# Kernel optimization log

Measured on AMD Instinct MI355X. Metric: run time of the kernel, lower is better.

The kernel has to match this reference:

```python
import jax, jax.numpy as jnp
import numpy as np

N_NODES = 90  # hard-coded per-graph node count in the original module
HIDDEN = 128


def setup_inputs() -> dict:
    key = jax.random.key(0)
    ks = jax.random.split(key, 12)
    B = 8192
    adj = jax.random.uniform(ks[0], (B, N_NODES, N_NODES), dtype=jnp.float32)
    s_in = 1.0 / np.sqrt(N_NODES)
    s_h = 1.0 / np.sqrt(HIDDEN)
    return {
        "adj": adj,
        "W_mlp0": jax.random.normal(ks[1], (N_NODES, HIDDEN), jnp.float32) * s_in,
        "b_mlp0": jax.random.normal(ks[2], (HIDDEN,), jnp.float32) * s_in,
        "W_mlp1": jax.random.normal(ks[3], (HIDDEN, HIDDEN), jnp.float32) * s_h,
        "b_mlp1": jax.random.normal(ks[4], (HIDDEN,), jnp.float32) * s_h,
        "W_mlp2": jax.random.normal(ks[5], (HIDDEN, HIDDEN), jnp.float32) * s_h,
        "b_mlp2": jax.random.normal(ks[6], (HIDDEN,), jnp.float32) * s_h,
        "W_res1": jax.random.normal(ks[7], (HIDDEN, HIDDEN), jnp.float32) * s_h,
        "b_res1": jax.random.normal(ks[8], (HIDDEN,), jnp.float32) * s_h,
        "W_res2": jax.random.normal(ks[9], (HIDDEN, HIDDEN), jnp.float32) * s_h,
        "b_res2": jax.random.normal(ks[10], (HIDDEN,), jnp.float32) * s_h,
    }


def reference(adj, W_mlp0, b_mlp0, W_mlp1, b_mlp1, W_mlp2, b_mlp2,
              W_res1, b_res1, W_res2, b_res2):
    B = adj.shape[0]
    # raw node features: identity per graph (torch.eye(90) concatenated)
    raw_x = jnp.broadcast_to(jnp.eye(N_NODES, dtype=adj.dtype), (B, N_NODES, N_NODES))

    def gconv(x, W, b):
        # block-diagonal Adj_block @ x == batched per-graph matmul, then linear
        return jnp.einsum('bij,bjk->bik', adj, x) @ W + b

    # encoding == 1 branch, layers = 3
    h0 = gconv(raw_x, W_mlp0, b_mlp0)                    # mlps[0](raw_x, A)
    r1 = h0 @ W_res1 + b_res1                            # res[1](h0)
    x = jax.nn.relu(gconv(h0, W_mlp1, b_mlp1)) + r1      # layer 1
    Y = jax.nn.relu(gconv(x, W_mlp2, b_mlp2) + (r1 @ W_res2 + b_res2))  # final

    # decoder: per-graph inner-product, concatenated along node axis
    Z = jnp.einsum('bik,bjk->bij', Y, Y)                 # [B, 90, 90]
    return Z.reshape(B * N_NODES, N_NODES)
```

## Files before the change

### kernel.cpp

```cpp
#include <hip/hip_runtime.h>
#include <hip/hip_bf16.h>


#define NN 90
#define HH 128
#define NT 256

typedef _Float16 half8 __attribute__((ext_vector_type(8)));
typedef _Float16 half4 __attribute__((ext_vector_type(4)));
typedef float floatx16 __attribute__((ext_vector_type(16)));

#define SR 136
#define SR8 17
#define ST 104
#define ST8 13
#define ST4 26

#define MFMA(a, b, c) __builtin_amdgcn_mfma_f32_32x32x16_f16((a), (b), (c), 0, 0, 0)

__global__ void prep_weights(const float* __restrict__ W0,
                             const float* __restrict__ Wr1,
                             const float* __restrict__ W1,
                             const float* __restrict__ W2,
                             const float* __restrict__ Wr2,
                             _Float16* __restrict__ ws)
{
    const int idx = blockIdx.x * blockDim.x + threadIdx.x;
    if (idx >= 77824) return;
    if (idx < 12288) {
        const int n = idx / 96, k = idx - n * 96;
        ws[idx] = (k < NN) ? (_Float16)W0[k * HH + n] : (_Float16)0.f;
    } else {
        const int j = idx - 12288;
        const int m = j >> 14;
        const int r = j & 16383;
        const int n = r >> 7, k = r & 127;
        const float* src = (m == 0) ? Wr1 : (m == 1) ? W1 : (m == 2) ? W2 : Wr2;
        ws[idx] = (_Float16)src[k * HH + n];
    }
}

__global__ __launch_bounds__(NT) void graphcnn_mfma(
    const float* __restrict__ adj,
    const _Float16* __restrict__ wts,
    const float* __restrict__ b0, const float* __restrict__ b1,
    const float* __restrict__ b2, const float* __restrict__ br1,
    const float* __restrict__ br2,
    float* __restrict__ out)
{
    __shared__ __align__(16) unsigned char smem[98816];
    _Float16* adjH = (_Float16*)smem;
    _Float16* bufA = (_Float16*)(smem + 19968);
    _Float16* bufT = (_Float16*)(smem + 46080);
    _Float16* r1R  = (_Float16*)(smem + 72704);

    const int t    = threadIdx.x;
    const int wv   = t >> 6;
    const int lane = t & 63;
    const int p    = lane & 31;
    const int h    = lane >> 5;
    const int n    = wv * 32 + p;

    const _Float16* W0T  = wts;
    const _Float16* Wr1T = wts + 12288;
    const _Float16* W1T  = Wr1T + 16384;
    const _Float16* W2T  = W1T + 16384;
    const _Float16* Wr2T = W2T + 16384;

    for (int i = t; i < (96 * ST) / 2; i += NT) ((unsigned int*)adjH)[i] = 0u;
    __syncthreads();
    const float* Ag = adj + (size_t)blockIdx.x * (NN * NN);
    for (int i = t; i < NN * NN; i += NT) {
        const int r = i / NN, c = i - r * NN;
        adjH[r * ST + c] = (_Float16)Ag[i];
    }
    __syncthreads();

    auto writeR = [&](_Float16* buf, int mt, int col, const floatx16& A) {
        #pragma unroll
        for (int r = 0; r < 16; r++) {
            const int node = mt * 32 + (r & 3) + 8 * (r >> 2) + 4 * h;
            buf[node * SR + col] = (_Float16)A[r];
        }
    };
    auto writeT = [&](_Float16* buf, int mt, int col, const floatx16& A) {
        #pragma unroll
        for (int rg = 0; rg < 4; rg++) {
            half4 v = { (_Float16)A[4*rg], (_Float16)A[4*rg+1],
                        (_Float16)A[4*rg+2], (_Float16)A[4*rg+3] };
            ((half4*)buf)[col * ST4 + mt * 8 + 2 * rg + h] = v;
        }
    };

    floatx16 acc0, acc1, acc2;

    {
        half8 bf[6];
        #pragma unroll
        for (int kt = 0; kt < 6; kt++) bf[kt] = ((const half8*)W0T)[n * 12 + kt * 2 + h];
        const float bias = b0[n];
        #pragma unroll
        for (int r = 0; r < 16; r++) { acc0[r] = bias; acc1[r] = bias; acc2[r] = bias; }
        #pragma unroll
        for (int kt = 0; kt < 6; kt++) {
            half8 a0 = ((const half8*)adjH)[(0 * 32 + p) * ST8 + kt * 2 + h];
            half8 a1 = ((const half8*)adjH)[(1 * 32 + p) * ST8 + kt * 2 + h];
            half8 a2 = ((const half8*)adjH)[(2 * 32 + p) * ST8 + kt * 2 + h];
            acc0 = MFMA(a0, bf[kt], acc0);
            acc1 = MFMA(a1, bf[kt], acc1);
            acc2 = MFMA(a2, bf[kt], acc2);
        }
        writeR(bufA, 0, n, acc0); writeR(bufA, 1, n, acc1); writeR(bufA, 2, n, acc2);
        writeT(bufT, 0, n, acc0); writeT(bufT, 1, n, acc1); writeT(bufT, 2, n, acc2);
    }
    __syncthreads();

    {
        half8 bf[8];
        #pragma unroll
        for (int kt = 0; kt < 8; kt++) bf[kt] = ((const half8*)Wr1T)[n * 16 + kt * 2 + h];
        const float bias = br1[n];
        #pragma unroll
        for (int r = 0; r < 16; r++) { acc0[r] = bias; acc1[r] = bias; acc2[r] = bias; }
        #pragma unroll
        for (int kt = 0; kt < 8; kt++) {
            half8 a0 = ((const half8*)bufA)[(0 * 32 + p) * SR8 + kt * 2 + h];
            half8 a1 = ((const half8*)bufA)[(1 * 32 + p) * SR8 + kt * 2 + h];
            half8 a2 = ((const half8*)bufA)[(2 * 32 + p) * SR8 + kt * 2 + h];
            acc0 = MFMA(a0, bf[kt], acc0);
            acc1 = MFMA(a1, bf[kt], acc1);
            acc2 = MFMA(a2, bf[kt], acc2);
        }
        writeR(r1R, 0, n, acc0); writeR(r1R, 1, n, acc1); writeR(r1R, 2, n, acc2);
    }
    __syncthreads();

    {
        #pragma unroll
        for (int r = 0; r < 16; r++) { acc0[r] = 0.f; acc1[r] = 0.f; acc2[r] = 0.f; }
        #pragma unroll
        for (int kt = 0; kt < 6; kt++) {
            half8 bfk = ((const half8*)bufT)[n * ST8 + kt * 2 + h];
            half8 a0 = ((const half8*)adjH)[(0 * 32 + p) * ST8 + kt * 2 + h];
            half8 a1 = ((const half8*)adjH)[(1 * 32 + p) * ST8 + kt * 2 + h];
            half8 a2 = ((const half8*)adjH)[(2 * 32 + p) * ST8 + kt * 2 + h];
            acc0 = MFMA(a0, bfk, acc0);
            acc1 = MFMA(a1, bfk, acc1);
            acc2 = MFMA(a2, bfk, acc2);
        }
        writeR(bufA, 0, n, acc0); writeR(bufA, 1, n, acc1); writeR(bufA, 2, n, acc2);
    }
    __syncthreads();

    {
        half8 bf[8];
        #pragma unroll
        for (int kt = 0; kt < 8; kt++) bf[kt] = ((const half8*)W1T)[n * 16 + kt * 2 + h];
        const float bias = b1[n];
        #pragma unroll
        for (int r = 0; r < 16; r++) { acc0[r] = bias; acc1[r] = bias; acc2[r] = bias; }
        #pragma unroll
        for (int kt = 0; kt < 8; kt++) {
            half8 a0 = ((const half8*)bufA)[(0 * 32 + p) * SR8 + kt * 2 + h];
            half8 a1 = ((const half8*)bufA)[(1 * 32 + p) * SR8 + kt * 2 + h];
            half8 a2 = ((const half8*)bufA)[(2 * 32 + p) * SR8 + kt * 2 + h];
            acc0 = MFMA(a0, bf[kt], acc0);
            acc1 = MFMA(a1, bf[kt], acc1);
            acc2 = MFMA(a2, bf[kt], acc2);
        }
        #pragma unroll
        for (int mt = 0; mt < 3; mt++) {
            floatx16& A = (mt == 0) ? acc0 : (mt == 1) ? acc1 : acc2;
            floatx16 xv;
            #pragma unroll
            for (int r = 0; r < 16; r++) {
                const int node = mt * 32 + (r & 3) + 8 * (r >> 2) + 4 * h;
                xv[r] = fmaxf(A[r], 0.f) + (float)r1R[node * SR + n];
            }
            writeT(bufT, mt, n, xv);
        }
    }
    __syncthreads();

    {
        #pragma unroll
        for (int r = 0; r < 16; r++) { acc0[r] = 0.f; acc1[r] = 0.f; acc2[r] = 0.f; }
        #pragma unroll
        for (int kt = 0; kt < 6; kt++) {
            half8 bfk = ((const half8*)bufT)[n * ST8 + kt * 2 + h];
            half8 a0 = ((const half8*)adjH)[(0 * 32 + p) * ST8 + kt * 2 + h];
            half8 a1 = ((const half8*)adjH)[(1 * 32 + p) * ST8 + kt * 2 + h];
            half8 a2 = ((const half8*)adjH)[(2 * 32 + p) * ST8 + kt * 2 + h];
            acc0 = MFMA(a0, bfk, acc0);
            acc1 = MFMA(a1, bfk, acc1);
            acc2 = MFMA(a2, bfk, acc2);
        }
        writeR(bufA, 0, n, acc0); writeR(bufA, 1, n, acc1); writeR(bufA, 2, n, acc2);
    }
    __syncthreads();

    {
        half8 bf[8];
        #pragma unroll
        for (int kt = 0; kt < 8; kt++) bf[kt] = ((const half8*)W2T)[n * 16 + kt * 2 + h];
        const float bias = b2[n] + br2[n];
        #pragma unroll
        for (int r = 0; r < 16; r++) { acc0[r] = bias; acc1[r] = bias; acc2[r] = bias; }
        #pragma unroll
        for (int kt = 0; kt < 8; kt++) {
            half8 a0 = ((const half8*)bufA)[(0 * 32 + p) * SR8 + kt * 2 + h];
            half8 a1 = ((const half8*)bufA)[(1 * 32 + p) * SR8 + kt * 2 + h];
            half8 a2 = ((const half8*)bufA)[(2 * 32 + p) * SR8 + kt * 2 + h];
            acc0 = MFMA(a0, bf[kt], acc0);
            acc1 = MFMA(a1, bf[kt], acc1);
            acc2 = MFMA(a2, bf[kt], acc2);
        }
        half8 bg[8];
        #pragma unroll
        for (int kt = 0; kt < 8; kt++) bg[kt] = ((const half8*)Wr2T)[n * 16 + kt * 2 + h];
        #pragma unroll
        for (int kt = 0; kt < 8; kt++) {
            half8 a0 = ((const half8*)r1R)[(0 * 32 + p) * SR8 + kt * 2 + h];
            half8 a1 = ((const half8*)r1R)[(1 * 32 + p) * SR8 + kt * 2 + h];
            half8 a2 = ((const half8*)r1R)[(2 * 32 + p) * SR8 + kt * 2 + h];
            acc0 = MFMA(a0, bg[kt], acc0);
            acc1 = MFMA(a1, bg[kt], acc1);
            acc2 = MFMA(a2, bg[kt], acc2);
        }
        _Float16* YR = bufT;
        #pragma unroll
        for (int mt = 0; mt < 3; mt++) {
            floatx16& A = (mt == 0) ? acc0 : (mt == 1) ? acc1 : acc2;
            #pragma unroll
            for (int r = 0; r < 16; r++) {
                const int node = mt * 32 + (r & 3) + 8 * (r >> 2) + 4 * h;
                YR[node * SR + n] = (_Float16)fmaxf(A[r], 0.f);
            }
        }
    }
    __syncthreads();

    {
        const _Float16* YR = bufT;
        float* outb = out + (size_t)blockIdx.x * (NN * NN);
        auto ztile = [&](int mt, int nt) {
            floatx16 acc;
            #pragma unroll
            for (int r = 0; r < 16; r++) acc[r] = 0.f;
            #pragma unroll
            for (int kt = 0; kt < 8; kt++) {
                half8 av = ((const half8*)YR)[(mt * 32 + p) * SR8 + kt * 2 + h];
                half8 bv = ((const half8*)YR)[(nt * 32 + p) * SR8 + kt * 2 + h];
                acc = MFMA(av, bv, acc);
            }
            const int col = nt * 32 + p;
            if (col < NN) {
                #pragma unroll
                for (int r = 0; r < 16; r++) {
                    const int row = mt * 32 + (r & 3) + 8 * (r >> 2) + 4 * h;
                    if (row < NN) outb[row * NN + col] = acc[r];
                }
            }
        };
        if      (wv == 0) { ztile(0, 0); ztile(0, 1); ztile(0, 2); }
        else if (wv == 1) { ztile(1, 0); ztile(1, 1); }
        else if (wv == 2) { ztile(1, 2); ztile(2, 0); }
        else              { ztile(2, 1); ztile(2, 2); }
    }
}

extern "C" void kernel_launch(void* const* d_in, const int* in_sizes, int n_in,
                              void* d_out, int out_size, void* d_ws, size_t ws_size,
                              hipStream_t stream) {
    const float* adj = (const float*)d_in[0];
    const float* W0  = (const float*)d_in[1];
    const float* b0  = (const float*)d_in[2];
    const float* W1  = (const float*)d_in[3];
    const float* b1  = (const float*)d_in[4];
    const float* W2  = (const float*)d_in[5];
    const float* b2  = (const float*)d_in[6];
    const float* Wr1 = (const float*)d_in[7];
    const float* br1 = (const float*)d_in[8];
    const float* Wr2 = (const float*)d_in[9];
    const float* br2 = (const float*)d_in[10];
    float* out = (float*)d_out;
    _Float16* wts = (_Float16*)d_ws;

    prep_weights<<<76, 1024, 0, stream>>>(W0, Wr1, W1, W2, Wr2, wts);

    const int B = in_sizes[0] / (NN * NN);
    graphcnn_mfma<<<B, NT, 0, stream>>>(adj, wts, b0, b1, b2, br1, br2, out);
}
```

Baseline: 819.7 us.

## Split per-graph work across 12 waves, one 32-row tile per wave

Raises the block from 4 to 12 waves so each wave owns one 32-row by 32-column output tile instead of three row tiles, and spreads the nine decoder tiles across nine waves. Each matmul now uses two independent accumulator chains to hide MFMA latency. The r1 residual is kept in registers instead of re-read from LDS, and extra barriers are added so in-place buffer overwrites stay safe. The cost is more barriers per stage, launch_bounds(768,3) register pressure, and redundant weight-fragment loads across the three row-tile waves.

```diff
diff --git a/kernel.cpp b/kernel.cpp
--- a/kernel.cpp
+++ b/kernel.cpp
@@ -4,7 +4,7 @@
 
 #define NN 90
 #define HH 128
-#define NT 256
+#define NT 768
 
 typedef _Float16 half8 __attribute__((ext_vector_type(8)));
 typedef _Float16 half4 __attribute__((ext_vector_type(4)));
@@ -40,7 +40,7 @@
     }
 }
 
-__global__ __launch_bounds__(NT) void graphcnn_mfma(
+__global__ __launch_bounds__(NT, 3) void graphcnn_mfma(
     const float* __restrict__ adj,
     const _Float16* __restrict__ wts,
     const float* __restrict__ b0, const float* __restrict__ b1,
@@ -59,7 +59,10 @@
     const int lane = t & 63;
     const int p    = lane & 31;
     const int h    = lane >> 5;
-    const int n    = wv * 32 + p;
+    const int mt   = wv >> 2;
+    const int cg   = wv & 3;
+    const int n    = cg * 32 + p;
+    const int arow = mt * 32 + p;
 
     const _Float16* W0T  = wts;
     const _Float16* Wr1T = wts + 12288;
@@ -76,42 +79,43 @@
     }
     __syncthreads();
 
-    auto writeR = [&](_Float16* buf, int mt, int col, const floatx16& A) {
+    auto ldA = [&](const _Float16* buf, int s8, int kt) {
+        return ((const half8*)buf)[arow * s8 + kt * 2 + h];
+    };
+    auto writeR = [&](_Float16* buf, const floatx16& A) {
         #pragma unroll
         for (int r = 0; r < 16; r++) {
             const int node = mt * 32 + (r & 3) + 8 * (r >> 2) + 4 * h;
-            buf[node * SR + col] = (_Float16)A[r];
+            buf[node * SR + n] = (_Float16)A[r];
         }
     };
-    auto writeT = [&](_Float16* buf, int mt, int col, const floatx16& A) {
+    auto writeT = [&](_Float16* buf, const floatx16& A) {
         #pragma unroll
         for (int rg = 0; rg < 4; rg++) {
             half4 v = { (_Float16)A[4*rg], (_Float16)A[4*rg+1],
                         (_Float16)A[4*rg+2], (_Float16)A[4*rg+3] };
-            ((half4*)buf)[col * ST4 + mt * 8 + 2 * rg + h] = v;
+            ((half4*)buf)[n * ST4 + mt * 8 + 2 * rg + h] = v;
         }
     };
 
-    floatx16 acc0, acc1, acc2;
+    floatx16 r1reg;
 
     {
         half8 bf[6];
         #pragma unroll
         for (int kt = 0; kt < 6; kt++) bf[kt] = ((const half8*)W0T)[n * 12 + kt * 2 + h];
         const float bias = b0[n];
-        #pragma unroll
-        for (int r = 0; r < 16; r++) { acc0[r] = bias; acc1[r] = bias; acc2[r] = bias; }
-        #pragma unroll
-        for (int kt = 0; kt < 6; kt++) {
-            half8 a0 = ((const half8*)adjH)[(0 * 32 + p) * ST8 + kt * 2 + h];
-            half8 a1 = ((const half8*)adjH)[(1 * 32 + p) * ST8 + kt * 2 + h];
-            half8 a2 = ((const half8*)adjH)[(2 * 32 + p) * ST8 + kt * 2 + h];
-            acc0 = MFMA(a0, bf[kt], acc0);
-            acc1 = MFMA(a1, bf[kt], acc1);
-            acc2 = MFMA(a2, bf[kt], acc2);
-        }
-        writeR(bufA, 0, n, acc0); writeR(bufA, 1, n, acc1); writeR(bufA, 2, n, acc2);
-        writeT(bufT, 0, n, acc0); writeT(bufT, 1, n, acc1); writeT(bufT, 2, n, acc2);
+        floatx16 ae, ao;
+        #pragma unroll
+        for (int r = 0; r < 16; r++) { ae[r] = bias; ao[r] = 0.f; }
+        #pragma unroll
+        for (int kt = 0; kt < 6; kt += 2) {
+            ae = MFMA(ldA(adjH, ST8, kt),     bf[kt],     ae);
+            ao = MFMA(ldA(adjH, ST8, kt + 1), bf[kt + 1], ao);
+        }
+        floatx16 acc = ae + ao;
+        writeR(bufA, acc);
+        writeT(bufT, acc);
     }
     __syncthreads();
 
@@ -120,35 +124,33 @@
         #pragma unroll
         for (int kt = 0; kt < 8; kt++) bf[kt] = ((const half8*)Wr1T)[n * 16 + kt * 2 + h];
         const float bias = br1[n];
-        #pragma unroll
-        for (int r = 0; r < 16; r++) { acc0[r] = bias; acc1[r] = bias; acc2[r] = bias; }
-        #pragma unroll
-        for (int kt = 0; kt < 8; kt++) {
-            half8 a0 = ((const half8*)bufA)[(0 * 32 + p) * SR8 + kt * 2 + h];
-            half8 a1 = ((const half8*)bufA)[(1 * 32 + p) * SR8 + kt * 2 + h];
-            half8 a2 = ((const half8*)bufA)[(2 * 32 + p) * SR8 + kt * 2 + h];
-            acc0 = MFMA(a0, bf[kt], acc0);
-            acc1 = MFMA(a1, bf[kt], acc1);
-            acc2 = MFMA(a2, bf[kt], acc2);
-        }
-        writeR(r1R, 0, n, acc0); writeR(r1R, 1, n, acc1); writeR(r1R, 2, n, acc2);
-    }
-    __syncthreads();
-
-    {
-        #pragma unroll
-        for (int r = 0; r < 16; r++) { acc0[r] = 0.f; acc1[r] = 0.f; acc2[r] = 0.f; }
-        #pragma unroll
-        for (int kt = 0; kt < 6; kt++) {
-            half8 bfk = ((const half8*)bufT)[n * ST8 + kt * 2 + h];
-            half8 a0 = ((const half8*)adjH)[(0 * 32 + p) * ST8 + kt * 2 + h];
-            half8 a1 = ((const half8*)adjH)[(1 * 32 + p) * ST8 + kt * 2 + h];
-            half8 a2 = ((const half8*)adjH)[(2 * 32 + p) * ST8 + kt * 2 + h];
-            acc0 = MFMA(a0, bfk, acc0);
-            acc1 = MFMA(a1, bfk, acc1);
-            acc2 = MFMA(a2, bfk, acc2);
-        }
-        writeR(bufA, 0, n, acc0); writeR(bufA, 1, n, acc1); writeR(bufA, 2, n, acc2);
+        floatx16 ae, ao;
+        #pragma unroll
+        for (int r = 0; r < 16; r++) { ae[r] = bias; ao[r] = 0.f; }
+        #pragma unroll
+        for (int kt = 0; kt < 8; kt += 2) {
+            ae = MFMA(ldA(bufA, SR8, kt),     bf[kt],     ae);
+            ao = MFMA(ldA(bufA, SR8, kt + 1), bf[kt + 1], ao);
+        }
+        r1reg = ae + ao;
+        writeR(r1R, r1reg);
+    }
+    __syncthreads();
+
+    {
+        floatx16 ae, ao;
+        #pragma unroll
+        for (int r = 0; r < 16; r++) { ae[r] = 0.f; ao[r] = 0.f; }
+        #pragma unroll
+        for (int kt = 0; kt < 6; kt += 2) {
+            half8 b0v = ((const half8*)bufT)[n * ST8 + kt * 2 + h];
+            half8 b1v = ((const half8*)bufT)[n * ST8 + (kt + 1) * 2 + h];
+            ae = MFMA(ldA(adjH, ST8, kt),     b0v, ae);
+            ao = MFMA(ldA(adjH, ST8, kt + 1), b1v, ao);
+        }
+        floatx16 acc = ae + ao;
+        __syncthreads();
+        writeR(bufA, acc);
     }
     __syncthreads();
 
@@ -157,115 +159,87 @@
         #pragma unroll
         for (int kt = 0; kt < 8; kt++) bf[kt] = ((const half8*)W1T)[n * 16 + kt * 2 + h];
         const float bias = b1[n];
-        #pragma unroll
-        for (int r = 0; r < 16; r++) { acc0[r] = bias; acc1[r] = bias; acc2[r] = bias; }
+        floatx16 ae, ao;
+        #pragma unroll
+        for (int r = 0; r < 16; r++) { ae[r] = bias; ao[r] = 0.f; }
+        #pragma unroll
+        for (int kt = 0; kt < 8; kt += 2) {
+            ae = MFMA(ldA(bufA, SR8, kt),     bf[kt],     ae);
+            ao = MFMA(ldA(bufA, SR8, kt + 1), bf[kt + 1], ao);
+        }
+        floatx16 xv;
+        #pragma unroll
+        for (int r = 0; r < 16; r++) xv[r] = fmaxf(ae[r] + ao[r], 0.f) + r1reg[r];
+        __syncthreads();
+        writeT(bufT, xv);
+    }
+    __syncthreads();
+
+    {
+        floatx16 ae, ao;
+        #pragma unroll
+        for (int r = 0; r < 16; r++) { ae[r] = 0.f; ao[r] = 0.f; }
+        #pragma unroll
+        for (int kt = 0; kt < 6; kt += 2) {
+            half8 b0v = ((const half8*)bufT)[n * ST8 + kt * 2 + h];
+            half8 b1v = ((const half8*)bufT)[n * ST8 + (kt + 1) * 2 + h];
+            ae = MFMA(ldA(adjH, ST8, kt),     b0v, ae);
+            ao = MFMA(ldA(adjH, ST8, kt + 1), b1v, ao);
+        }
+        floatx16 acc = ae + ao;
+        __syncthreads();
+        writeR(bufA, acc);
+    }
+    __syncthreads();
+
+    {
+        half8 bf[8], bg[8];
         #pragma unroll
         for (int kt = 0; kt < 8; kt++) {
-            half8 a0 = ((const half8*)bufA)[(0 * 32 + p) * SR8 + kt * 2 + h];
-            half8 a1 = ((const half8*)bufA)[(1 * 32 + p) * SR8 + kt * 2 + h];
-            half8 a2 = ((const half8*)bufA)[(2 * 32 + p) * SR8 + kt * 2 + h];
-            acc0 = MFMA(a0, bf[kt], acc0);
-            acc1 = MFMA(a1, bf[kt], acc1);
-            acc2 = MFMA(a2, bf[kt], acc2);
-        }
-        #pragma unroll
-        for (int mt = 0; mt < 3; mt++) {
-            floatx16& A = (mt == 0) ? acc0 : (mt == 1) ? acc1 : acc2;
-            floatx16 xv;
+            bf[kt] = ((const half8*)W2T)[n * 16 + kt * 2 + h];
+            bg[kt] = ((const half8*)Wr2T)[n * 16 + kt * 2 + h];
+        }
+        const float bias = b2[n] + br2[n];
+        floatx16 au, ar;
+        #pragma unroll
+        for (int r = 0; r < 16; r++) { au[r] = bias; ar[r] = 0.f; }
+        #pragma unroll
+        for (int kt = 0; kt < 8; kt++) {
+            au = MFMA(ldA(bufA, SR8, kt), bf[kt], au);
+            ar = MFMA(ldA(r1R,  SR8, kt), bg[kt], ar);
+        }
+        floatx16 yv;
+        #pragma unroll
+        for (int r = 0; r < 16; r++) yv[r] = fmaxf(au[r] + ar[r], 0.f);
+        __syncthreads();
+        writeR(bufT, yv);
+    }
+    __syncthreads();
+
+    if (wv < 9) {
+        const _Float16* YR = bufT;
+        const int zm = wv / 3, zn = wv - zm * 3;
+        float* outb = out + (size_t)blockIdx.x * (NN * NN);
+        floatx16 ze, zo;
+        #pragma unroll
+        for (int r = 0; r < 16; r++) { ze[r] = 0.f; zo[r] = 0.f; }
+        #pragma unroll
+        for (int kt = 0; kt < 8; kt += 2) {
+            half8 av0 = ((const half8*)YR)[(zm * 32 + p) * SR8 + kt * 2 + h];
+            half8 bv0 = ((const half8*)YR)[(zn * 32 + p) * SR8 + kt * 2 + h];
+            half8 av1 = ((const half8*)YR)[(zm * 32 + p) * SR8 + (kt + 1) * 2 + h];
+            half8 bv1 = ((const half8*)YR)[(zn * 32 + p) * SR8 + (kt + 1) * 2 + h];
+            ze = MFMA(av0, bv0, ze);
+            zo = MFMA(av1, bv1, zo);
+        }
+        const int col = zn * 32 + p;
+        if (col < NN) {
             #pragma unroll
             for (int r = 0; r < 16; r++) {
-                const int node = mt * 32 + (r & 3) + 8 * (r >> 2) + 4 * h;
-                xv[r] = fmaxf(A[r], 0.f) + (float)r1R[node * SR + n];
+                const int row = zm * 32 + (r & 3) + 8 * (r >> 2) + 4 * h;
+                if (row < NN) outb[row * NN + col] = ze[r] + zo[r];
             }
-            writeT(bufT, mt, n, xv);
-        }
-    }
-    __syncthreads();
-
-    {
-        #pragma unroll
-        for (int r = 0; r < 16; r++) { acc0[r] = 0.f; acc1[r] = 0.f; acc2[r] = 0.f; }
-        #pragma unroll
-        for (int kt = 0; kt < 6; kt++) {
-            half8 bfk = ((const half8*)bufT)[n * ST8 + kt * 2 + h];
-            half8 a0 = ((const half8*)adjH)[(0 * 32 + p) * ST8 + kt * 2 + h];
-            half8 a1 = ((const half8*)adjH)[(1 * 32 + p) * ST8 + kt * 2 + h];
-            half8 a2 = ((const half8*)adjH)[(2 * 32 + p) * ST8 + kt * 2 + h];
-            acc0 = MFMA(a0, bfk, acc0);
-            acc1 = MFMA(a1, bfk, acc1);
-            acc2 = MFMA(a2, bfk, acc2);
-        }
-        writeR(bufA, 0, n, acc0); writeR(bufA, 1, n, acc1); writeR(bufA, 2, n, acc2);
-    }
-    __syncthreads();
-
-    {
-        half8 bf[8];
-        #pragma unroll
-        for (int kt = 0; kt < 8; kt++) bf[kt] = ((const half8*)W2T)[n * 16 + kt * 2 + h];
-        const float bias = b2[n] + br2[n];
-        #pragma unroll
-        for (int r = 0; r < 16; r++) { acc0[r] = bias; acc1[r] = bias; acc2[r] = bias; }
-        #pragma unroll
-        for (int kt = 0; kt < 8; kt++) {
-            half8 a0 = ((const half8*)bufA)[(0 * 32 + p) * SR8 + kt * 2 + h];
-            half8 a1 = ((const half8*)bufA)[(1 * 32 + p) * SR8 + kt * 2 + h];
-            half8 a2 = ((const half8*)bufA)[(2 * 32 + p) * SR8 + kt * 2 + h];
-            acc0 = MFMA(a0, bf[kt], acc0);
-            acc1 = MFMA(a1, bf[kt], acc1);
-            acc2 = MFMA(a2, bf[kt], acc2);
-        }
-        half8 bg[8];
-        #pragma unroll
-        for (int kt = 0; kt < 8; kt++) bg[kt] = ((const half8*)Wr2T)[n * 16 + kt * 2 + h];
-        #pragma unroll
-        for (int kt = 0; kt < 8; kt++) {
-            half8 a0 = ((const half8*)r1R)[(0 * 32 + p) * SR8 + kt * 2 + h];
-            half8 a1 = ((const half8*)r1R)[(1 * 32 + p) * SR8 + kt * 2 + h];
-            half8 a2 = ((const half8*)r1R)[(2 * 32 + p) * SR8 + kt * 2 + h];
-            acc0 = MFMA(a0, bg[kt], acc0);
-            acc1 = MFMA(a1, bg[kt], acc1);
-            acc2 = MFMA(a2, bg[kt], acc2);
-        }
-        _Float16* YR = bufT;
-        #pragma unroll
-        for (int mt = 0; mt < 3; mt++) {
-            floatx16& A = (mt == 0) ? acc0 : (mt == 1) ? acc1 : acc2;
-            #pragma unroll
-            for (int r = 0; r < 16; r++) {
-                const int node = mt * 32 + (r & 3) + 8 * (r >> 2) + 4 * h;
-                YR[node * SR + n] = (_Float16)fmaxf(A[r], 0.f);
-            }
-        }
-    }
-    __syncthreads();
-
-    {
-        const _Float16* YR = bufT;
-        float* outb = out + (size_t)blockIdx.x * (NN * NN);
-        auto ztile = [&](int mt, int nt) {
-            floatx16 acc;
-            #pragma unroll
-            for (int r = 0; r < 16; r++) acc[r] = 0.f;
-            #pragma unroll
-            for (int kt = 0; kt < 8; kt++) {
-                half8 av = ((const half8*)YR)[(mt * 32 + p) * SR8 + kt * 2 + h];
-                half8 bv = ((const half8*)YR)[(nt * 32 + p) * SR8 + kt * 2 + h];
-                acc = MFMA(av, bv, acc);
-            }
-            const int col = nt * 32 + p;
-            if (col < NN) {
-                #pragma unroll
-                for (int r = 0; r < 16; r++) {
-                    const int row = mt * 32 + (r & 3) + 8 * (r >> 2) + 4 * h;
-                    if (row < NN) outb[row * NN + col] = acc[r];
-                }
-            }
-        };
-        if      (wv == 0) { ztile(0, 0); ztile(0, 1); ztile(0, 2); }
-        else if (wv == 1) { ztile(1, 0); ztile(1, 1); }
-        else if (wv == 2) { ztile(1, 2); ztile(2, 0); }
-        else              { ztile(2, 1); ztile(2, 2); }
+        }
     }
 }
 
```

New measurement: 1.042 ms. 1.27x slower.
